# Kernel tuning notes

Measured on AMD Instinct MI355X. Metric: run time of the kernel, lower is better.

Reference implementation:

```python
import jax, jax.numpy as jnp
import numpy as np

EMBED = 1024
HEADS = 16
HEAD_DIM = EMBED // HEADS
B, S = 2, 2048


def setup_inputs() -> dict:
    key = jax.random.key(0)
    k1, k2, k3 = jax.random.split(key, 3)
    scale = 1.0 / np.sqrt(EMBED)
    x = jax.random.normal(k1, (B, S, EMBED), dtype=jnp.float32)
    mask = jnp.ones((B, 1, 1, S), dtype=jnp.int32)
    Wqkv = jax.random.normal(k2, (3 * EMBED, EMBED), dtype=jnp.float32) * scale
    bqkv = jnp.zeros((3 * EMBED,), dtype=jnp.float32)
    Wout = jax.random.normal(k3, (EMBED, EMBED), dtype=jnp.float32) * scale
    bout = jnp.zeros((EMBED,), dtype=jnp.float32)
    return {"x": x, "mask": mask, "Wqkv": Wqkv, "bqkv": bqkv, "Wout": Wout, "bout": bout}


def reference(x, mask, Wqkv, bqkv, Wout, bout):
    Bsz, Sl, E = x.shape
    # fused QKV projection (torch Linear: x @ W.T + b)
    qkv = x @ Wqkv.T + bqkv                      # [B, S, 3E]
    qkv = qkv.reshape(Bsz, Sl, 3, HEADS, HEAD_DIM)
    qkv = jnp.transpose(qkv, (0, 2, 3, 1, 4))    # [B, 3, H, S, D]
    q, k, v = qkv[:, 0], qkv[:, 1], qkv[:, 2]    # each [B, H, S, D]
    scores = jnp.einsum("bhqd,bhkd->bhqk", q, k) / np.sqrt(HEAD_DIM)
    scores = jnp.where(mask == 0, -jnp.inf, scores)  # mask broadcasts [B,1,1,S]
    attn = jax.nn.softmax(scores, axis=-1)       # dropout is identity at eval
    out = jnp.einsum("bhqk,bhkd->bhqd", attn, v) # [B, H, S, D]
    out = jnp.transpose(out, (0, 2, 1, 3)).reshape(Bsz, Sl, E)
    return out @ Wout.T + bout
```

## Files before the change

### kernel.cpp

```cpp
#include <hip/hip_runtime.h>
#include <stdint.h>

typedef unsigned short u16;
typedef __bf16  bf16x8 __attribute__((ext_vector_type(8)));
typedef u16     u16x8  __attribute__((ext_vector_type(8)));
typedef u16     u16x4  __attribute__((ext_vector_type(4)));
typedef float   f32x4  __attribute__((ext_vector_type(4)));

#define MFMA16x16x32(a, b, c) __builtin_amdgcn_mfma_f32_16x16x32_bf16((a), (b), (c), 0, 0, 0)

__device__ __forceinline__ u16 f2bf(float f) {
  uint32_t u = __float_as_uint(f);
  u += 0x7FFFu + ((u >> 16) & 1u);
  return (u16)(u >> 16);
}

__device__ __forceinline__ uint32_t pk2bf(float a, float b) {
  return (uint32_t)f2bf(a) | ((uint32_t)f2bf(b) << 16);
}

__device__ __forceinline__ bf16x8 ldfrag(const u16* p) {
  return __builtin_bit_cast(bf16x8, *(const u16x8*)p);
}

__device__ __forceinline__ void gl2lds16(const u16* g, u16* l) {
  __builtin_amdgcn_global_load_lds(
      (__attribute__((address_space(1))) void*)g,
      (__attribute__((address_space(3))) void*)l, 16, 0, 0);
}

__global__ __launch_bounds__(256) void convert3(
    const float* __restrict__ x, const float* __restrict__ wq,
    const float* __restrict__ wo, u16* __restrict__ xb,
    u16* __restrict__ wqb, u16* __restrict__ wob) {
  const int NX = (4096 * 1024) / 8;
  const int NQ = (3072 * 1024) / 8;
  int i = blockIdx.x * 256 + threadIdx.x;
  const float* s;
  u16* d;
  if (i < NX)           { s = x;  d = xb;  }
  else if (i < NX + NQ) { s = wq; d = wqb; i -= NX; }
  else                  { s = wo; d = wob; i -= NX + NQ; }
  f32x4 a = ((const f32x4*)s)[2 * (size_t)i];
  f32x4 b = ((const f32x4*)s)[2 * (size_t)i + 1];
  u16x8 r;
  #pragma unroll
  for (int e = 0; e < 4; ++e) { r[e] = f2bf(a[e]); r[4 + e] = f2bf(b[e]); }
  ((u16x8*)d)[i] = r;
}

__global__ __launch_bounds__(256) void qkv_gemm(
    const u16* __restrict__ A, const u16* __restrict__ Bw,
    const float* __restrict__ bias, u16* __restrict__ Qo,
    u16* __restrict__ Ko, u16* __restrict__ Vto) {
  __shared__ __align__(16) u16 As[128 * 32];
  __shared__ __align__(16) u16 Bs[128 * 32];

  const int t = threadIdx.x;
  const int lane = t & 63, w = t >> 6;
  const int quad = lane >> 4, col = lane & 15;
  const int wm = w & 1, wn = w >> 1;
  const int m0 = blockIdx.y * 128, n0 = blockIdx.x * 128;

  f32x4 acc[4][4] = {};

  const int ar = t >> 2, ac = (t & 3) * 8;
  const u16* Ag0 = A + (size_t)(m0 + ar) * 1024 + ac;
  const u16* Ag1 = Ag0 + 64 * 1024;
  const u16* Bg0 = Bw + (size_t)(n0 + ar) * 1024 + ac;
  const u16* Bg1 = Bg0 + 64 * 1024;
  u16* Al0 = As + t * 8;
  u16* Al1 = As + 2048 + t * 8;
  u16* Bl0 = Bs + t * 8;
  u16* Bl1 = Bs + 2048 + t * 8;

  for (int kt = 0; kt < 32; ++kt) {
    const int ko = kt * 32;
    __syncthreads();
    gl2lds16(Ag0 + ko, Al0);
    gl2lds16(Ag1 + ko, Al1);
    gl2lds16(Bg0 + ko, Bl0);
    gl2lds16(Bg1 + ko, Bl1);
    __syncthreads();

    bf16x8 bfr[4];
    #pragma unroll
    for (int j = 0; j < 4; ++j)
      bfr[j] = ldfrag(Bs + (wn * 64 + j * 16 + col) * 32 + quad * 8);
    #pragma unroll
    for (int i = 0; i < 4; ++i) {
      bf16x8 afr = ldfrag(As + (wm * 64 + i * 16 + col) * 32 + quad * 8);
      #pragma unroll
      for (int j = 0; j < 4; ++j)
        acc[i][j] = MFMA16x16x32(afr, bfr[j], acc[i][j]);
    }
  }

  #pragma unroll
  for (int i = 0; i < 4; ++i) {
    const int m = m0 + wm * 64 + i * 16 + quad * 4;
    const int bb = m >> 11;
    const int s = m & 2047;
    #pragma unroll
    for (int j = 0; j < 4; ++j) {
      const int n = n0 + wn * 64 + j * 16 + col;
      const float bv = bias[n];
      const int which = n >> 10;
      const int h = (n >> 6) & 15;
      const int d = n & 63;
      if (which == 2) {
        u16x4 vv;
        #pragma unroll
        for (int r = 0; r < 4; ++r) vv[r] = f2bf(acc[i][j][r] + bv);
        *(u16x4*)(Vto + ((size_t)(bb * 16 + h) * 64 + d) * 2048 + s) = vv;
      } else {
        u16* dst = (which == 0) ? Qo : Ko;
        const float scale = (which == 0) ? 0.125f : 1.0f;
        const size_t base = ((size_t)(bb * 16 + h) * 2048 + s) * 64 + d;
        #pragma unroll
        for (int r = 0; r < 4; ++r)
          dst[base + (size_t)r * 64] = f2bf((acc[i][j][r] + bv) * scale);
      }
    }
  }
}

__global__ __launch_bounds__(512, 4) void attn(
    const u16* __restrict__ Q, const u16* __restrict__ K,
    const u16* __restrict__ Vt, const int* __restrict__ mask,
    u16* __restrict__ AO) {
  __shared__ __align__(16) u16 Ks[128 * 64];
  __shared__ __align__(16) u16 Vs[64 * 128];
  __shared__ __align__(16) u16 Ps[8][16 * 136];

  const int t = threadIdx.x;
  const int lane = t & 63, w = t >> 6;
  const int quad = lane >> 4, col = lane & 15;
  const int qb = blockIdx.x, bh = blockIdx.y;
  const int b = bh >> 4, h = bh & 15;

  const u16* Qh = Q + (size_t)bh * (2048 * 64);
  const u16* Kh = K + (size_t)bh * (2048 * 64);
  const u16* Vh = Vt + (size_t)bh * (64 * 2048);
  const int* mb = mask + b * 2048;

  const int q = qb * 128 + w * 16 + col;
  bf16x8 aQ[2];
  aQ[0] = ldfrag(Qh + (size_t)q * 64 + quad * 8);
  aQ[1] = ldfrag(Qh + (size_t)q * 64 + 32 + quad * 8);

  f32x4 o[4] = {};
  float l = 0.f;
  u16* Pw = &Ps[w][0];

  for (int kb = 0; kb < 16; ++kb) {
    const int key0 = kb * 128;
    __syncthreads();
    #pragma unroll
    for (int p = 0; p < 2; ++p) {
      int c = t + 512 * p;
      int kr = c >> 3, kc = c & 7;
      gl2lds16(Kh + (size_t)(key0 + kr) * 64 + (kc ^ (kr & 7)) * 8, Ks + c * 8);
      int vr = c >> 4, vc = c & 15;
      gl2lds16(Vh + (size_t)vr * 2048 + key0 + (vc ^ (vr & 15)) * 8, Vs + c * 8);
    }
    __syncthreads();

    f32x4 sc[8] = {};
    #pragma unroll
    for (int j = 0; j < 8; ++j) {
      #pragma unroll
      for (int kh = 0; kh < 2; ++kh) {
        bf16x8 ak = ldfrag(Ks + (j * 16 + col) * 64 + (((kh * 4 + quad) ^ (col & 7)) * 8));
        sc[j] = MFMA16x16x32(ak, aQ[kh], sc[j]);
      }
    }

    #pragma unroll
    for (int j = 0; j < 8; ++j) {
      int4 m4 = *(const int4*)(mb + key0 + j * 16 + quad * 4);
      float p0 = m4.x ? __expf(sc[j][0]) : 0.f;
      float p1 = m4.y ? __expf(sc[j][1]) : 0.f;
      float p2 = m4.z ? __expf(sc[j][2]) : 0.f;
      float p3 = m4.w ? __expf(sc[j][3]) : 0.f;
      l += (p0 + p1) + (p2 + p3);
      uint2 pk;
      pk.x = pk2bf(p0, p1);
      pk.y = pk2bf(p2, p3);
      *(uint2*)(Pw + col * 136 + j * 16 + quad * 4) = pk;
    }

    #pragma unroll
    for (int jp = 0; jp < 4; ++jp) {
      bf16x8 bP = ldfrag(Pw + col * 136 + jp * 32 + quad * 8);
      #pragma unroll
      for (int dt = 0; dt < 4; ++dt) {
        bf16x8 av = ldfrag(Vs + (dt * 16 + col) * 128 + (((jp * 4 + quad) ^ col) * 8));
        o[dt] = MFMA16x16x32(av, bP, o[dt]);
      }
    }
  }

  l += __shfl_xor(l, 16);
  l += __shfl_xor(l, 32);
  const float rl = 1.0f / l;

  #pragma unroll
  for (int dt = 0; dt < 4; ++dt) {
    u16x4 v;
    #pragma unroll
    for (int r = 0; r < 4; ++r) v[r] = f2bf(o[dt][r] * rl);
    *(u16x4*)(AO + (size_t)(b * 2048 + q) * 1024 + h * 64 + dt * 16 + quad * 4) = v;
  }
}

__global__ __launch_bounds__(256) void proj_gemm(
    const u16* __restrict__ A, const u16* __restrict__ Bw,
    const float* __restrict__ bias, float* __restrict__ out) {
  __shared__ __align__(16) u16 As[128 * 32];
  __shared__ __align__(16) u16 Bs[128 * 32];

  const int t = threadIdx.x;
  const int lane = t & 63, w = t >> 6;
  const int quad = lane >> 4, col = lane & 15;
  const int wm = w & 1, wn = w >> 1;
  const int m0 = blockIdx.y * 128, n0 = blockIdx.x * 128;

  f32x4 acc[4][4] = {};

  const int ar = t >> 2, ac = (t & 3) * 8;
  const u16* Ag0 = A + (size_t)(m0 + ar) * 1024 + ac;
  const u16* Ag1 = Ag0 + 64 * 1024;
  const u16* Bg0 = Bw + (size_t)(n0 + ar) * 1024 + ac;
  const u16* Bg1 = Bg0 + 64 * 1024;
  u16* Al0 = As + t * 8;
  u16* Al1 = As + 2048 + t * 8;
  u16* Bl0 = Bs + t * 8;
  u16* Bl1 = Bs + 2048 + t * 8;

  for (int kt = 0; kt < 32; ++kt) {
    const int ko = kt * 32;
    __syncthreads();
    gl2lds16(Ag0 + ko, Al0);
    gl2lds16(Ag1 + ko, Al1);
    gl2lds16(Bg0 + ko, Bl0);
    gl2lds16(Bg1 + ko, Bl1);
    __syncthreads();

    bf16x8 bfr[4];
    #pragma unroll
    for (int j = 0; j < 4; ++j)
      bfr[j] = ldfrag(Bs + (wn * 64 + j * 16 + col) * 32 + quad * 8);
    #pragma unroll
    for (int i = 0; i < 4; ++i) {
      bf16x8 afr = ldfrag(As + (wm * 64 + i * 16 + col) * 32 + quad * 8);
      #pragma unroll
      for (int j = 0; j < 4; ++j)
        acc[i][j] = MFMA16x16x32(afr, bfr[j], acc[i][j]);
    }
  }

  #pragma unroll
  for (int i = 0; i < 4; ++i) {
    const int m = m0 + wm * 64 + i * 16 + quad * 4;
    #pragma unroll
    for (int j = 0; j < 4; ++j) {
      const int n = n0 + wn * 64 + j * 16 + col;
      const float bv = bias[n];
      #pragma unroll
      for (int r = 0; r < 4; ++r)
        out[(size_t)(m + r) * 1024 + n] = acc[i][j][r] + bv;
    }
  }
}

extern "C" void kernel_launch(void* const* d_in, const int* in_sizes, int n_in,
                              void* d_out, int out_size, void* d_ws, size_t ws_size,
                              hipStream_t stream) {
  (void)in_sizes; (void)n_in; (void)out_size; (void)ws_size;
  const float* x    = (const float*)d_in[0];
  const int*   mask = (const int*)d_in[1];
  const float* Wqkv = (const float*)d_in[2];
  const float* bqkv = (const float*)d_in[3];
  const float* Wout = (const float*)d_in[4];
  const float* bout = (const float*)d_in[5];
  float* out = (float*)d_out;
  char* ws = (char*)d_ws;

  u16* Xb  = (u16*)(ws);
  u16* Wqb = (u16*)(ws + ((size_t)8  << 20));
  u16* Wob = (u16*)(ws + ((size_t)14 << 20));
  u16* Qb  = (u16*)(ws + ((size_t)16 << 20));
  u16* Kb  = (u16*)(ws + ((size_t)24 << 20));
  u16* Vtb = (u16*)(ws + ((size_t)32 << 20));
  u16* AO  = Xb;

  convert3<<<dim3(4096), dim3(256), 0, stream>>>(x, Wqkv, Wout, Xb, Wqb, Wob);
  qkv_gemm<<<dim3(24, 32), dim3(256), 0, stream>>>(Xb, Wqb, bqkv, Qb, Kb, Vtb);
  attn<<<dim3(16, 32), dim3(512), 0, stream>>>(Qb, Kb, Vtb, mask, AO);
  proj_gemm<<<dim3(8, 32), dim3(256), 0, stream>>>(AO, Wob, bout, out);
}
```

Before: 233.1 us.

## Process two query tiles per wave in attention, halving threads per block

The attention kernel now runs 4 waves per block instead of 8, with each wave handling 32 query rows as two 16-row tiles. Each K and V fragment read from LDS therefore feeds two MFMAs, cutting LDS read traffic per unit of work. The P staging is split into two half-passes of 64 keys each, so the per-wave scratch stays small. The bf16 rounding of P is replaced by truncation through a byte-permute, with the mask applied as a bitwise AND, and the row sum is accumulated from the truncated values so it stays consistent with the PV product. The cost is higher register pressure, fewer waves per block, and slightly lower precision for P.

```diff
diff --git a/kernel.cpp b/kernel.cpp
--- a/kernel.cpp
+++ b/kernel.cpp
@@ -15,8 +15,8 @@
   return (u16)(u >> 16);
 }
 
-__device__ __forceinline__ uint32_t pk2bf(float a, float b) {
-  return (uint32_t)f2bf(a) | ((uint32_t)f2bf(b) << 16);
+__device__ __forceinline__ uint32_t pktrunc(float a, float b) {
+  return __builtin_amdgcn_perm(__float_as_uint(b), __float_as_uint(a), 0x07060302u);
 }
 
 __device__ __forceinline__ bf16x8 ldfrag(const u16* p) {
@@ -125,13 +125,13 @@
   }
 }
 
-__global__ __launch_bounds__(512, 4) void attn(
+__global__ __launch_bounds__(256, 2) void attn(
     const u16* __restrict__ Q, const u16* __restrict__ K,
     const u16* __restrict__ Vt, const int* __restrict__ mask,
     u16* __restrict__ AO) {
   __shared__ __align__(16) u16 Ks[128 * 64];
   __shared__ __align__(16) u16 Vs[64 * 128];
-  __shared__ __align__(16) u16 Ps[8][16 * 136];
+  __shared__ __align__(16) u16 Ps[4][32 * 68];
 
   const int t = threadIdx.x;
   const int lane = t & 63, w = t >> 6;
@@ -144,21 +144,25 @@
   const u16* Vh = Vt + (size_t)bh * (64 * 2048);
   const int* mb = mask + b * 2048;
 
-  const int q = qb * 128 + w * 16 + col;
-  bf16x8 aQ[2];
-  aQ[0] = ldfrag(Qh + (size_t)q * 64 + quad * 8);
-  aQ[1] = ldfrag(Qh + (size_t)q * 64 + 32 + quad * 8);
-
-  f32x4 o[4] = {};
-  float l = 0.f;
+  const int qw = qb * 128 + w * 32;
+  bf16x8 aQ[2][2];
+  #pragma unroll
+  for (int ct = 0; ct < 2; ++ct) {
+    #pragma unroll
+    for (int kh = 0; kh < 2; ++kh)
+      aQ[ct][kh] = ldfrag(Qh + (size_t)(qw + ct * 16 + col) * 64 + kh * 32 + quad * 8);
+  }
+
+  f32x4 o[2][4] = {};
+  float l[2] = {0.f, 0.f};
   u16* Pw = &Ps[w][0];
 
   for (int kb = 0; kb < 16; ++kb) {
     const int key0 = kb * 128;
     __syncthreads();
     #pragma unroll
-    for (int p = 0; p < 2; ++p) {
-      int c = t + 512 * p;
+    for (int p = 0; p < 4; ++p) {
+      int c = t + 256 * p;
       int kr = c >> 3, kc = c & 7;
       gl2lds16(Kh + (size_t)(key0 + kr) * 64 + (kc ^ (kr & 7)) * 8, Ks + c * 8);
       int vr = c >> 4, vc = c & 15;
@@ -166,51 +170,69 @@
     }
     __syncthreads();
 
-    f32x4 sc[8] = {};
+    f32x4 sc[2][8] = {};
     #pragma unroll
     for (int j = 0; j < 8; ++j) {
       #pragma unroll
       for (int kh = 0; kh < 2; ++kh) {
         bf16x8 ak = ldfrag(Ks + (j * 16 + col) * 64 + (((kh * 4 + quad) ^ (col & 7)) * 8));
-        sc[j] = MFMA16x16x32(ak, aQ[kh], sc[j]);
+        sc[0][j] = MFMA16x16x32(ak, aQ[0][kh], sc[0][j]);
+        sc[1][j] = MFMA16x16x32(ak, aQ[1][kh], sc[1][j]);
       }
     }
 
     #pragma unroll
-    for (int j = 0; j < 8; ++j) {
-      int4 m4 = *(const int4*)(mb + key0 + j * 16 + quad * 4);
-      float p0 = m4.x ? __expf(sc[j][0]) : 0.f;
-      float p1 = m4.y ? __expf(sc[j][1]) : 0.f;
-      float p2 = m4.z ? __expf(sc[j][2]) : 0.f;
-      float p3 = m4.w ? __expf(sc[j][3]) : 0.f;
-      l += (p0 + p1) + (p2 + p3);
-      uint2 pk;
-      pk.x = pk2bf(p0, p1);
-      pk.y = pk2bf(p2, p3);
-      *(uint2*)(Pw + col * 136 + j * 16 + quad * 4) = pk;
-    }
-
-    #pragma unroll
-    for (int jp = 0; jp < 4; ++jp) {
-      bf16x8 bP = ldfrag(Pw + col * 136 + jp * 32 + quad * 8);
-      #pragma unroll
-      for (int dt = 0; dt < 4; ++dt) {
-        bf16x8 av = ldfrag(Vs + (dt * 16 + col) * 128 + (((jp * 4 + quad) ^ col) * 8));
-        o[dt] = MFMA16x16x32(av, bP, o[dt]);
+    for (int hp = 0; hp < 2; ++hp) {
+      #pragma unroll
+      for (int jj = 0; jj < 4; ++jj) {
+        const int j = hp * 4 + jj;
+        int4 m4 = *(const int4*)(mb + key0 + j * 16 + quad * 4);
+        uint32_t M01 = (m4.x ? 0x0000FFFFu : 0u) | (m4.y ? 0xFFFF0000u : 0u);
+        uint32_t M23 = (m4.z ? 0x0000FFFFu : 0u) | (m4.w ? 0xFFFF0000u : 0u);
+        #pragma unroll
+        for (int ct = 0; ct < 2; ++ct) {
+          uint32_t pkA = pktrunc(__expf(sc[ct][j][0]), __expf(sc[ct][j][1])) & M01;
+          uint32_t pkB = pktrunc(__expf(sc[ct][j][2]), __expf(sc[ct][j][3])) & M23;
+          l[ct] += (__uint_as_float(pkA << 16) + __uint_as_float(pkA & 0xFFFF0000u)) +
+                   (__uint_as_float(pkB << 16) + __uint_as_float(pkB & 0xFFFF0000u));
+          uint2 pk; pk.x = pkA; pk.y = pkB;
+          *(uint2*)(Pw + (ct * 16 + col) * 68 + jj * 16 + quad * 4) = pk;
+        }
       }
-    }
-  }
-
-  l += __shfl_xor(l, 16);
-  l += __shfl_xor(l, 32);
-  const float rl = 1.0f / l;
-
-  #pragma unroll
-  for (int dt = 0; dt < 4; ++dt) {
-    u16x4 v;
-    #pragma unroll
-    for (int r = 0; r < 4; ++r) v[r] = f2bf(o[dt][r] * rl);
-    *(u16x4*)(AO + (size_t)(b * 2048 + q) * 1024 + h * 64 + dt * 16 + quad * 4) = v;
+
+      #pragma unroll
+      for (int jp = 0; jp < 2; ++jp) {
+        const int gw = hp * 2 + jp;
+        bf16x8 bP0 = ldfrag(Pw + col * 68 + jp * 32 + quad * 8);
+        bf16x8 bP1 = ldfrag(Pw + (16 + col) * 68 + jp * 32 + quad * 8);
+        #pragma unroll
+        for (int dt = 0; dt < 4; ++dt) {
+          bf16x8 av = ldfrag(Vs + (dt * 16 + col) * 128 + (((gw * 4 + quad) ^ col) * 8));
+          o[0][dt] = MFMA16x16x32(av, bP0, o[0][dt]);
+          o[1][dt] = MFMA16x16x32(av, bP1, o[1][dt]);
+        }
+      }
+    }
+  }
+
+  #pragma unroll
+  for (int ct = 0; ct < 2; ++ct) {
+    float s = l[ct];
+    s += __shfl_xor(s, 16);
+    s += __shfl_xor(s, 32);
+    l[ct] = 1.0f / s;
+  }
+
+  #pragma unroll
+  for (int ct = 0; ct < 2; ++ct) {
+    const int q = qw + ct * 16 + col;
+    #pragma unroll
+    for (int dt = 0; dt < 4; ++dt) {
+      u16x4 v;
+      #pragma unroll
+      for (int r = 0; r < 4; ++r) v[r] = f2bf(o[ct][dt][r] * l[ct]);
+      *(u16x4*)(AO + (size_t)(b * 2048 + q) * 1024 + h * 64 + dt * 16 + quad * 4) = v;
+    }
   }
 }
 
@@ -297,6 +319,6 @@
 
   convert3<<<dim3(4096), dim3(256), 0, stream>>>(x, Wqkv, Wout, Xb, Wqb, Wob);
   qkv_gemm<<<dim3(24, 32), dim3(256), 0, stream>>>(Xb, Wqb, bqkv, Qb, Kb, Vtb);
-  attn<<<dim3(16, 32), dim3(512), 0, stream>>>(Qb, Kb, Vtb, mask, AO);
+  attn<<<dim3(16, 32), dim3(256), 0, stream>>>(Qb, Kb, Vtb, mask, AO);
   proj_gemm<<<dim3(8, 32), dim3(256), 0, stream>>>(AO, Wob, bout, out);
 }
```

Measured after the change: 243.7 us. +4.5%, slower.
